# Kernel tuning notes

Measured on AMD Instinct MI355X. Metric: run time of the kernel, lower is better.

Reference implementation:

```python
import jax, jax.numpy as jnp
import numpy as np

N, E_RAW, IN_DIM, OUT_DIM, HEADS, EDGE_DIM = 20000, 320000, 64, 64, 4, 1
NEG_SLOPE = 0.2  # PyG GATv2 default negative_slope
LN_EPS = 1e-5


def setup_inputs() -> dict:
    key = jax.random.key(0)
    ks = jax.random.split(key, 14)
    HD = HEADS * OUT_DIM
    s_in = 1.0 / np.sqrt(IN_DIM)
    s_hd = 1.0 / np.sqrt(HD)
    return {
        "x": jax.random.normal(ks[0], (N, IN_DIM), dtype=jnp.float32),
        "edge_index": jax.random.randint(ks[1], (2, E_RAW), 0, N, dtype=jnp.int64),
        "edge_attr": jax.random.normal(ks[2], (E_RAW, EDGE_DIM), dtype=jnp.float32),
        # GATv2Conv params: lin_l, lin_r (with bias), lin_edge (no bias), att, final bias
        "W_l": jax.random.normal(ks[3], (IN_DIM, HD), dtype=jnp.float32) * s_in,
        "b_l": jnp.zeros((HD,), dtype=jnp.float32),
        "W_r": jax.random.normal(ks[4], (IN_DIM, HD), dtype=jnp.float32) * s_in,
        "b_r": jnp.zeros((HD,), dtype=jnp.float32),
        "W_e": jax.random.normal(ks[5], (EDGE_DIM, HD), dtype=jnp.float32),
        "att": jax.random.normal(ks[6], (HEADS, OUT_DIM), dtype=jnp.float32) * (1.0 / np.sqrt(OUT_DIM)),
        "bias_conv": jnp.zeros((HD,), dtype=jnp.float32),
        # proj: Linear(heads*out_dim -> out_dim)
        "W_p": jax.random.normal(ks[7], (HD, OUT_DIM), dtype=jnp.float32) * s_hd,
        "b_p": jnp.zeros((OUT_DIM,), dtype=jnp.float32),
        # LayerNorm(out_dim)
        "gamma": jnp.ones((OUT_DIM,), dtype=jnp.float32),
        "beta": jnp.zeros((OUT_DIM,), dtype=jnp.float32),
    }


def _gat_block(x, edge_index, edge_attr, W_l, b_l, W_r, b_r, W_e, att,
               bias_conv, W_p, b_p, gamma, beta):
    n = x.shape[0]
    H, D = att.shape
    # add self loops; edge_attr for loops = mean of existing (fill_value='mean')
    loop = jnp.arange(n)
    src = jnp.concatenate([edge_index[0], loop])
    dst = jnp.concatenate([edge_index[1], loop])
    ea_mean = jnp.mean(edge_attr, axis=0, keepdims=True)
    ea = jnp.concatenate([edge_attr, jnp.broadcast_to(ea_mean, (n, edge_attr.shape[1]))], axis=0)
    # node transforms: [N, H, D]
    x_l = (x @ W_l + b_l).reshape(n, H, D)
    x_r = (x @ W_r + b_r).reshape(n, H, D)
    e_feat = (ea @ W_e).reshape(-1, H, D)          # [Etot, H, D]
    # GATv2 attention logits per edge/head
    m = jax.nn.leaky_relu(x_l[src] + x_r[dst] + e_feat, NEG_SLOPE)
    logits = jnp.einsum('ehd,hd->eh', m, att)      # [Etot, H]
    # scatter-softmax over incoming edges of each target node
    lmax = jax.ops.segment_max(logits, dst, num_segments=n)
    lmax = jnp.where(jnp.isfinite(lmax), lmax, 0.0)
    ex = jnp.exp(logits - lmax[dst])
    den = jax.ops.segment_sum(ex, dst, num_segments=n)
    alpha = ex / (den[dst] + 1e-16)                # [Etot, H]
    # aggregate: sum_j alpha_ij * x_l[j]
    out = jax.ops.segment_sum(alpha[:, :, None] * x_l[src], dst, num_segments=n)
    h = out.reshape(n, H * D) + bias_conv
    # proj + residual + ELU + LayerNorm (dropout inactive in eval)
    h = h @ W_p + b_p
    h = h + x
    h = jax.nn.elu(h)
    mu = jnp.mean(h, axis=-1, keepdims=True)
    var = jnp.mean(jnp.square(h - mu), axis=-1, keepdims=True)
    return (h - mu) * jax.lax.rsqrt(var + LN_EPS) * gamma + beta


def reference(x, edge_index, edge_attr, W_l, b_l, W_r, b_r, W_e, att,
              bias_conv, W_p, b_p, gamma, beta):
    return _gat_block(x, edge_index, edge_attr, W_l, b_l, W_r, b_r, W_e, att,
                      bias_conv, W_p, b_p, gamma, beta)
```

## Files before the change

### kernel.cpp

```cpp
#include <hip/hip_runtime.h>
#include <math.h>

typedef _Float16 h2 __attribute__((ext_vector_type(2)));
typedef _Float16 h4 __attribute__((ext_vector_type(4)));
typedef _Float16 h8 __attribute__((ext_vector_type(8)));
typedef float f8 __attribute__((ext_vector_type(8)));

#define NEG_SLOPE 0.2f
#define LN_EPS 1e-5f
#define RESCALE_THR 8.0f
#define SLOT 64

#if __has_builtin(__builtin_amdgcn_fdot2)
#define FDOT2(a, b, c) __builtin_amdgcn_fdot2((a), (b), (c), false)
#else
static __device__ __forceinline__ float FDOT2(h2 a, h2 b, float c) {
    return c + (float)a[0] * (float)b[0] + (float)a[1] * (float)b[1];
}
#endif

static __device__ __forceinline__ float red8_dpp(float p) {
    p += __int_as_float(__builtin_amdgcn_mov_dpp(__float_as_int(p), 0xB1, 0xF, 0xF, true));
    p += __int_as_float(__builtin_amdgcn_mov_dpp(__float_as_int(p), 0x4E, 0xF, 0xF, true));
    p += __int_as_float(__builtin_amdgcn_mov_dpp(__float_as_int(p), 0x141, 0xF, 0xF, true));
    return p;
}

static __device__ __forceinline__ _Float16 f16_bits(unsigned short u) {
    union { unsigned short u; _Float16 h; } c; c.u = u; return c.h;
}
static __device__ __forceinline__ unsigned short bits_f16(_Float16 h) {
    union { unsigned short u; _Float16 h; } c; c.h = h; return c.u;
}

__global__ void init_kernel(int* __restrict__ cursor, float* __restrict__ partials,
                            float* __restrict__ easum, int n, int eb) {
    int i = blockIdx.x * 256 + threadIdx.x;
    if (i < n) cursor[i] = 0;
    if (i < eb) partials[i] = 0.f;
    if (i == 0) easum[0] = 0.f;
}

__global__ __launch_bounds__(256) void fill_kernel(
    const int* __restrict__ ei, const float* __restrict__ ea,
    int* __restrict__ cursor, unsigned int* __restrict__ rec,
    float* __restrict__ partials, int E) {
    int i = blockIdx.x * 256 + threadIdx.x;
    float s = 0.f;
    if (i < E) {
        int src = ei[i];
        int dst = ei[E + i];
        float a = ea[i];
        s = a;
        int pos = atomicAdd(&cursor[dst], 1);
        if (pos < SLOT) {
            unsigned int pk = ((unsigned int)bits_f16((_Float16)a) << 16) | (unsigned int)src;
            rec[(size_t)dst * SLOT + pos] = pk;
        }
    }
    __shared__ float red[4];
#pragma unroll
    for (int o = 32; o >= 1; o >>= 1) s += __shfl_xor(s, o);
    if ((threadIdx.x & 63) == 0) red[threadIdx.x >> 6] = s;
    __syncthreads();
    if (threadIdx.x == 0) partials[blockIdx.x] = red[0] + red[1] + red[2] + red[3];
}

__global__ __launch_bounds__(256) void transform_kernel(
    const float* __restrict__ x, const float* __restrict__ Wl, const float* __restrict__ bl,
    const float* __restrict__ Wr, const float* __restrict__ br,
    _Float16* __restrict__ xlh, _Float16* __restrict__ xrh,
    const float* __restrict__ partials, float* __restrict__ easum,
    int n, int eb, float inv_e) {
    __shared__ float xs[8][64];
    int nb = blockIdx.x * 8;
    int rows = n - nb; if (rows > 8) rows = 8;
    int t = threadIdx.x;
    if (t < rows * 16) ((float4*)xs)[t] = ((const float4*)(x + (size_t)nb * 64))[t];
    __syncthreads();
    float blv = bl[t], brv = br[t];
    float accl[8], accr[8];
#pragma unroll
    for (int i = 0; i < 8; ++i) { accl[i] = blv; accr[i] = brv; }
    for (int k = 0; k < 64; k += 4) {
        float wl0 = Wl[(k + 0) * 256 + t], wl1 = Wl[(k + 1) * 256 + t];
        float wl2 = Wl[(k + 2) * 256 + t], wl3 = Wl[(k + 3) * 256 + t];
        float wr0 = Wr[(k + 0) * 256 + t], wr1 = Wr[(k + 1) * 256 + t];
        float wr2 = Wr[(k + 2) * 256 + t], wr3 = Wr[(k + 3) * 256 + t];
#pragma unroll
        for (int i = 0; i < 8; ++i) {
            float4 xv = *(const float4*)&xs[i][k];
            accl[i] += xv.x * wl0 + xv.y * wl1 + xv.z * wl2 + xv.w * wl3;
            accr[i] += xv.x * wr0 + xv.y * wr1 + xv.z * wr2 + xv.w * wr3;
        }
    }
    for (int i = 0; i < rows; ++i) {
        xlh[(size_t)(nb + i) * 256 + t] = (_Float16)accl[i];
        xrh[(size_t)(nb + i) * 256 + t] = (_Float16)accr[i];
    }
    if (blockIdx.x == 0) {
        float s = 0.f;
        for (int i = t; i < eb; i += 256) s += partials[i];
#pragma unroll
        for (int o = 32; o >= 1; o >>= 1) s += __shfl_xor(s, o);
        __shared__ float red[4];
        if ((t & 63) == 0) red[t >> 6] = s;
        __syncthreads();
        if (t == 0) easum[0] = (red[0] + red[1] + red[2] + red[3]) * inv_e;
    }
}

__global__ __launch_bounds__(256) void gat_kernel(
    const _Float16* __restrict__ xlh, const _Float16* __restrict__ xrh,
    const int* __restrict__ cursor, const unsigned int* __restrict__ rec,
    const float* __restrict__ att, const float* __restrict__ We, const float* __restrict__ bias_conv,
    const float* __restrict__ easum, _Float16* __restrict__ hg, int n) {
    int wid = (blockIdx.x * blockDim.x + threadIdx.x) >> 6;
    if (wid >= n) return;
    int lane = threadIdx.x & 63;
    int half = lane >> 5, s = lane & 31;

    int pkv = (int)rec[(size_t)wid * SLOT + lane];
    int cnt = cursor[wid]; if (cnt > SLOT) cnt = SLOT;

    h8 xrv = ((const h8*)xrh)[(size_t)wid * 32 + s];
    h2 xr2[4], we2[4], c02 = {(_Float16)NEG_SLOPE, (_Float16)NEG_SLOPE};
    float atf[8];
    const float* attp = att + 8 * s;
    const float* wep = We + 8 * s;
#pragma unroll
    for (int j = 0; j < 4; ++j) {
        xr2[j] = (h2){xrv[2 * j], xrv[2 * j + 1]};
        we2[j] = (h2){(_Float16)wep[2 * j], (_Float16)wep[2 * j + 1]};
        atf[2 * j] = attp[2 * j]; atf[2 * j + 1] = attp[2 * j + 1];
    }
    const h8* xl8 = (const h8*)xlh;

    auto edge_p = [&](h8 v, _Float16 ah) -> float {
        h2 a2 = {ah, ah};
        float p = 0.f;
#pragma unroll
        for (int j = 0; j < 4; ++j) {
            h2 vj = (h2){v[2 * j], v[2 * j + 1]};
            h2 m = a2 * we2[j] + (vj + xr2[j]);
            h2 l = __builtin_elementwise_max(m, m * c02);
            p = fmaf((float)l[0], atf[2 * j], p);
            p = fmaf((float)l[1], atf[2 * j + 1], p);
        }
        return red8_dpp(p);
    };

    float M = -1e30f, S = 0.f;
    f8 accv = (f8)0.f;

#define ACC_FMA(V, W)                                        \
    _Pragma("unroll")                                        \
    for (int j = 0; j < 8; ++j) accv[j] = fmaf((float)(V)[j], (W), accv[j]);

#define ONLINE(P, V) {                                       \
        float newM = fmaxf(M, (P));                          \
        float sc = __expf(M - newM), w = __expf((P) - newM); \
        S = S * sc + w;                                      \
        accv *= sc;                                          \
        ACC_FMA(V, w);                                       \
        M = newM; }

#define LOADE(D, R)                                                         \
    int pk##D = __shfl(pkv, (R) + 2 * (D) + half);                          \
    h8 v##D = xl8[(size_t)(unsigned)(pk##D & 0xFFFF) * 32 + s];
#define PCOMP(D) float p##D = edge_p(v##D, f16_bits((unsigned short)((unsigned)pk##D >> 16)));

    {
        int pk0 = __shfl(pkv, 0);
        int src = wid;
        _Float16 ah = (_Float16)easum[0];
        if (half == 1 && cnt >= 1) {
            src = pk0 & 0xFFFF;
            ah = f16_bits((unsigned short)((unsigned)pk0 >> 16));
        }
        h8 v = xl8[(size_t)src * 32 + s];
        float p = edge_p(v, ah);
        if (half == 0 || cnt >= 1) {
            M = p; S = 1.f;
#pragma unroll
            for (int j = 0; j < 8; ++j) accv[j] = (float)v[j];
        }
    }
    int r = 1;
    for (; r + 15 < cnt; r += 16) {
        LOADE(0, r) LOADE(1, r) LOADE(2, r) LOADE(3, r)
        LOADE(4, r) LOADE(5, r) LOADE(6, r) LOADE(7, r)
        PCOMP(0) PCOMP(1) PCOMP(2) PCOMP(3)
        PCOMP(4) PCOMP(5) PCOMP(6) PCOMP(7)
        float pm = fmaxf(fmaxf(fmaxf(p0, p1), fmaxf(p2, p3)),
                         fmaxf(fmaxf(p4, p5), fmaxf(p6, p7)));
        if (__all(pm <= M + RESCALE_THR)) {
            float w0 = __expf(p0 - M), w1 = __expf(p1 - M);
            float w2 = __expf(p2 - M), w3 = __expf(p3 - M);
            float w4 = __expf(p4 - M), w5 = __expf(p5 - M);
            float w6 = __expf(p6 - M), w7 = __expf(p7 - M);
            S += ((w0 + w1) + (w2 + w3)) + ((w4 + w5) + (w6 + w7));
            ACC_FMA(v0, w0); ACC_FMA(v1, w1); ACC_FMA(v2, w2); ACC_FMA(v3, w3);
            ACC_FMA(v4, w4); ACC_FMA(v5, w5); ACC_FMA(v6, w6); ACC_FMA(v7, w7);
        } else {
            ONLINE(p0, v0); ONLINE(p1, v1); ONLINE(p2, v2); ONLINE(p3, v3);
            ONLINE(p4, v4); ONLINE(p5, v5); ONLINE(p6, v6); ONLINE(p7, v7);
        }
    }
    for (; r + 7 < cnt; r += 8) {
        LOADE(0, r) LOADE(1, r) LOADE(2, r) LOADE(3, r)
        PCOMP(0) PCOMP(1) PCOMP(2) PCOMP(3)
        float pm = fmaxf(fmaxf(p0, p1), fmaxf(p2, p3));
        if (__all(pm <= M + RESCALE_THR)) {
            float w0 = __expf(p0 - M), w1 = __expf(p1 - M);
            float w2 = __expf(p2 - M), w3 = __expf(p3 - M);
            S += (w0 + w1) + (w2 + w3);
            ACC_FMA(v0, w0); ACC_FMA(v1, w1); ACC_FMA(v2, w2); ACC_FMA(v3, w3);
        } else {
            ONLINE(p0, v0); ONLINE(p1, v1); ONLINE(p2, v2); ONLINE(p3, v3);
        }
    }
    for (; r + 1 < cnt; r += 2) {
        int pk0 = __shfl(pkv, r + half);
        h8 v0 = xl8[(size_t)(unsigned)(pk0 & 0xFFFF) * 32 + s];
        PCOMP(0)
        ONLINE(p0, v0);
    }
    if (r < cnt) {
        int pk0 = __shfl(pkv, r);
        h8 v0 = xl8[(size_t)(unsigned)(pk0 & 0xFFFF) * 32 + s];
        float p0 = edge_p(v0, f16_bits((unsigned short)((unsigned)pk0 >> 16)));
        if (half == 0) ONLINE(p0, v0);
    }

    float Mo = __shfl_xor(M, 32);
    float newM = fmaxf(M, Mo);
    float sc = __expf(M - newM);
    S *= sc;
    S += __shfl_xor(S, 32);
    accv *= sc;
#pragma unroll
    for (int j = 0; j < 8; ++j) accv[j] += __shfl_xor(accv[j], 32);
    float inv = 1.f / (S + 1e-16f);

    float4 bc = ((const float4*)bias_conv)[2 * s + half];
    int jb = 4 * half;
    h4 ov = {(_Float16)(accv[jb + 0] * inv + bc.x), (_Float16)(accv[jb + 1] * inv + bc.y),
             (_Float16)(accv[jb + 2] * inv + bc.z), (_Float16)(accv[jb + 3] * inv + bc.w)};
    ((h4*)hg)[(size_t)wid * 64 + 2 * s + half] = ov;
#undef ACC_FMA
#undef ONLINE
#undef LOADE
#undef PCOMP
}

__global__ __launch_bounds__(256) void proj_ln_kernel(
    const _Float16* __restrict__ hg, const float* __restrict__ Wp, const float* __restrict__ bp,
    const float* __restrict__ x, const float* __restrict__ gamma, const float* __restrict__ beta,
    float* __restrict__ out, int n) {
    __shared__ _Float16 wp_t[64 * 256];
    __shared__ _Float16 hs[32][264];
    int t = threadIdx.x;
    int nb = blockIdx.x * 32;
    for (int idx = t; idx < 4096; idx += 256) {
        float4 wv = ((const float4*)Wp)[idx];
        int k = idx >> 4, c0s = (idx & 15) * 4;
#pragma unroll
        for (int m = 0; m < 4; ++m) {
            int c = c0s + m;
            int off = c * 256 + ((((k >> 3) ^ ((c >> 2) & 7)) << 3) | (k & 7));
            wp_t[off] = (_Float16)((&wv.x)[m]);
        }
    }
    for (int idx = t; idx < 1024; idx += 256) {
        int row = idx >> 5, c8 = idx & 31;
        h8 hv = (h8)(_Float16)0.f;
        if (nb + row < n) hv = ((const h8*)hg)[(size_t)(nb + row) * 32 + c8];
        *(h8*)&hs[row][c8 * 8] = hv;
    }
    __syncthreads();

    int ng = t >> 4, cg = t & 15;
    int n0 = ng * 2, c0 = cg * 4;
    float acc[2][4];
#pragma unroll
    for (int a = 0; a < 2; ++a)
#pragma unroll
        for (int c = 0; c < 4; ++c) acc[a][c] = 0.f;

    for (int k = 0; k < 256; k += 8) {
        h8 hr[2], wr_[4];
#pragma unroll
        for (int a = 0; a < 2; ++a) hr[a] = *(const h8*)&hs[n0 + a][k];
#pragma unroll
        for (int j = 0; j < 4; ++j) {
            int c = c0 + j;
            int off = c * 256 + (((k >> 3) ^ ((c >> 2) & 7)) << 3);
            wr_[j] = *(const h8*)&wp_t[off];
        }
#pragma unroll
        for (int a = 0; a < 2; ++a) {
            const h2* hp = (const h2*)&hr[a];
#pragma unroll
            for (int j = 0; j < 4; ++j) {
                const h2* wp2 = (const h2*)&wr_[j];
                acc[a][j] = FDOT2(hp[0], wp2[0], acc[a][j]);
                acc[a][j] = FDOT2(hp[1], wp2[1], acc[a][j]);
                acc[a][j] = FDOT2(hp[2], wp2[2], acc[a][j]);
                acc[a][j] = FDOT2(hp[3], wp2[3], acc[a][j]);
            }
        }
    }

    float4 bpv = ((const float4*)bp)[cg];
    float4 gv  = ((const float4*)gamma)[cg];
    float4 bv  = ((const float4*)beta)[cg];
#pragma unroll
    for (int a = 0; a < 2; ++a) {
        int node = nb + n0 + a;
        float4 xv = make_float4(0.f, 0.f, 0.f, 0.f);
        if (node < n) xv = ((const float4*)x)[(size_t)node * 16 + cg];
        float h[4];
        h[0] = acc[a][0] + bpv.x + xv.x; h[1] = acc[a][1] + bpv.y + xv.y;
        h[2] = acc[a][2] + bpv.z + xv.z; h[3] = acc[a][3] + bpv.w + xv.w;
#pragma unroll
        for (int c = 0; c < 4; ++c) h[c] = h[c] > 0.f ? h[c] : expm1f(h[c]);
        float sum = h[0] + h[1] + h[2] + h[3];
#pragma unroll
        for (int o = 8; o >= 1; o >>= 1) sum += __shfl_xor(sum, o);
        float mu = sum * (1.f / 64.f);
        float d[4]; float s2 = 0.f;
#pragma unroll
        for (int c = 0; c < 4; ++c) { d[c] = h[c] - mu; s2 += d[c] * d[c]; }
#pragma unroll
        for (int o = 8; o >= 1; o >>= 1) s2 += __shfl_xor(s2, o);
        float r = rsqrtf(s2 * (1.f / 64.f) + LN_EPS);
        float4 ov;
        ov.x = d[0] * r * gv.x + bv.x; ov.y = d[1] * r * gv.y + bv.y;
        ov.z = d[2] * r * gv.z + bv.z; ov.w = d[3] * r * gv.w + bv.w;
        if (node < n) ((float4*)out)[(size_t)node * 16 + cg] = ov;
    }
}

extern "C" void kernel_launch(void* const* d_in, const int* in_sizes, int n_in,
                              void* d_out, int out_size, void* d_ws, size_t ws_size,
                              hipStream_t stream) {
    const float* x         = (const float*)d_in[0];
    const int*   ei        = (const int*)d_in[1];
    const float* ea        = (const float*)d_in[2];
    const float* Wl        = (const float*)d_in[3];
    const float* bl        = (const float*)d_in[4];
    const float* Wr        = (const float*)d_in[5];
    const float* br        = (const float*)d_in[6];
    const float* We        = (const float*)d_in[7];
    const float* att       = (const float*)d_in[8];
    const float* bias_conv = (const float*)d_in[9];
    const float* Wp        = (const float*)d_in[10];
    const float* bp        = (const float*)d_in[11];
    const float* gamma     = (const float*)d_in[12];
    const float* beta      = (const float*)d_in[13];
    float* out = (float*)d_out;

    int N = in_sizes[0] / 64;
    int E = in_sizes[2];
    int EB = (E + 255) / 256;

    char* w = (char*)d_ws;
    auto alloc = [&](size_t bytes) {
        char* p = w;
        w += (bytes + 255) & ~(size_t)255;
        return p;
    };
    _Float16*     xlh     = (_Float16*)    alloc((size_t)N * 256 * 2);
    _Float16*     xrh     = (_Float16*)    alloc((size_t)N * 256 * 2);
    _Float16*     hgh     = (_Float16*)    alloc((size_t)N * 256 * 2);
    unsigned int* rec     = (unsigned int*)alloc((size_t)N * SLOT * 4);
    int*          cursor  = (int*)         alloc((size_t)N * 4);
    float*        partials= (float*)       alloc((size_t)EB * 4);
    float*        easum   = (float*)       alloc(4);

    init_kernel<<<(N + 255) / 256, 256, 0, stream>>>(cursor, partials, easum, N, EB);
    fill_kernel<<<EB, 256, 0, stream>>>(ei, ea, cursor, rec, partials, E);
    transform_kernel<<<(N + 7) / 8, 256, 0, stream>>>(x, Wl, bl, Wr, br, xlh, xrh,
                                                      partials, easum, N, EB, 1.f / (float)E);
    gat_kernel<<<(N + 3) / 4, 256, 0, stream>>>(xlh, xrh, cursor, rec, att, We,
                                                bias_conv, easum, hgh, N);
    proj_ln_kernel<<<(N + 31) / 32, 256, 0, stream>>>(hgh, Wp, bp, x, gamma, beta, out, N);
}
```

Baseline: 108.2 us.

## Merge edge fill and node transform into one launch; widen proj block

The edge-bucketing fill and the node linear transform are independent, so they now run as one kernel whose blocks pick a role by block index. This lets both run at once instead of back to back. The edge_attr mean reduction moves into a small single-block kernel. The projection/LayerNorm kernel now uses 512 threads and 64 rows per block, which halves how often Wp is reloaded into LDS per row but needs more LDS per block. The proj compute section is not shown, so whether it was adapted to 512 threads cannot be checked.

```diff
diff --git a/kernel.cpp b/kernel.cpp
--- a/kernel.cpp
+++ b/kernel.cpp
@@ -33,81 +33,79 @@
     union { unsigned short u; _Float16 h; } c; c.h = h; return c.u;
 }
 
-__global__ void init_kernel(int* __restrict__ cursor, float* __restrict__ partials,
-                            float* __restrict__ easum, int n, int eb) {
+__global__ void init_kernel(int* __restrict__ cursor, int n) {
     int i = blockIdx.x * 256 + threadIdx.x;
     if (i < n) cursor[i] = 0;
-    if (i < eb) partials[i] = 0.f;
-    if (i == 0) easum[0] = 0.f;
-}
-
-__global__ __launch_bounds__(256) void fill_kernel(
+}
+
+__global__ __launch_bounds__(256) void prep_kernel(
     const int* __restrict__ ei, const float* __restrict__ ea,
-    int* __restrict__ cursor, unsigned int* __restrict__ rec,
-    float* __restrict__ partials, int E) {
-    int i = blockIdx.x * 256 + threadIdx.x;
-    float s = 0.f;
-    if (i < E) {
-        int src = ei[i];
-        int dst = ei[E + i];
-        float a = ea[i];
-        s = a;
-        int pos = atomicAdd(&cursor[dst], 1);
-        if (pos < SLOT) {
-            unsigned int pk = ((unsigned int)bits_f16((_Float16)a) << 16) | (unsigned int)src;
-            rec[(size_t)dst * SLOT + pos] = pk;
-        }
-    }
-    __shared__ float red[4];
-#pragma unroll
-    for (int o = 32; o >= 1; o >>= 1) s += __shfl_xor(s, o);
-    if ((threadIdx.x & 63) == 0) red[threadIdx.x >> 6] = s;
-    __syncthreads();
-    if (threadIdx.x == 0) partials[blockIdx.x] = red[0] + red[1] + red[2] + red[3];
-}
-
-__global__ __launch_bounds__(256) void transform_kernel(
+    int* __restrict__ cursor, unsigned int* __restrict__ rec, float* __restrict__ partials,
     const float* __restrict__ x, const float* __restrict__ Wl, const float* __restrict__ bl,
     const float* __restrict__ Wr, const float* __restrict__ br,
     _Float16* __restrict__ xlh, _Float16* __restrict__ xrh,
-    const float* __restrict__ partials, float* __restrict__ easum,
-    int n, int eb, float inv_e) {
-    __shared__ float xs[8][64];
-    int nb = blockIdx.x * 8;
-    int rows = n - nb; if (rows > 8) rows = 8;
-    int t = threadIdx.x;
-    if (t < rows * 16) ((float4*)xs)[t] = ((const float4*)(x + (size_t)nb * 64))[t];
-    __syncthreads();
-    float blv = bl[t], brv = br[t];
-    float accl[8], accr[8];
-#pragma unroll
-    for (int i = 0; i < 8; ++i) { accl[i] = blv; accr[i] = brv; }
-    for (int k = 0; k < 64; k += 4) {
-        float wl0 = Wl[(k + 0) * 256 + t], wl1 = Wl[(k + 1) * 256 + t];
-        float wl2 = Wl[(k + 2) * 256 + t], wl3 = Wl[(k + 3) * 256 + t];
-        float wr0 = Wr[(k + 0) * 256 + t], wr1 = Wr[(k + 1) * 256 + t];
-        float wr2 = Wr[(k + 2) * 256 + t], wr3 = Wr[(k + 3) * 256 + t];
-#pragma unroll
-        for (int i = 0; i < 8; ++i) {
-            float4 xv = *(const float4*)&xs[i][k];
-            accl[i] += xv.x * wl0 + xv.y * wl1 + xv.z * wl2 + xv.w * wl3;
-            accr[i] += xv.x * wr0 + xv.y * wr1 + xv.z * wr2 + xv.w * wr3;
-        }
-    }
-    for (int i = 0; i < rows; ++i) {
-        xlh[(size_t)(nb + i) * 256 + t] = (_Float16)accl[i];
-        xrh[(size_t)(nb + i) * 256 + t] = (_Float16)accr[i];
-    }
-    if (blockIdx.x == 0) {
+    int N, int E, int EB) {
+    int b = blockIdx.x, t = threadIdx.x;
+    if (b < EB) {
+        int i = b * 256 + t;
         float s = 0.f;
-        for (int i = t; i < eb; i += 256) s += partials[i];
+        if (i < E) {
+            int src = ei[i];
+            int dst = ei[E + i];
+            float a = ea[i];
+            s = a;
+            int pos = atomicAdd(&cursor[dst], 1);
+            if (pos < SLOT) {
+                unsigned int pk = ((unsigned int)bits_f16((_Float16)a) << 16) | (unsigned int)src;
+                rec[(size_t)dst * SLOT + pos] = pk;
+            }
+        }
+        __shared__ float red[4];
 #pragma unroll
         for (int o = 32; o >= 1; o >>= 1) s += __shfl_xor(s, o);
-        __shared__ float red[4];
         if ((t & 63) == 0) red[t >> 6] = s;
         __syncthreads();
-        if (t == 0) easum[0] = (red[0] + red[1] + red[2] + red[3]) * inv_e;
-    }
+        if (t == 0) partials[b] = red[0] + red[1] + red[2] + red[3];
+    } else {
+        __shared__ float xs[8][64];
+        int nb = (b - EB) * 8;
+        int rows = N - nb; if (rows > 8) rows = 8;
+        if (rows <= 0) return;
+        if (t < rows * 16) ((float4*)xs)[t] = ((const float4*)(x + (size_t)nb * 64))[t];
+        __syncthreads();
+        float blv = bl[t], brv = br[t];
+        float accl[8], accr[8];
+#pragma unroll
+        for (int i = 0; i < 8; ++i) { accl[i] = blv; accr[i] = brv; }
+        for (int k = 0; k < 64; k += 4) {
+            float wl0 = Wl[(k + 0) * 256 + t], wl1 = Wl[(k + 1) * 256 + t];
+            float wl2 = Wl[(k + 2) * 256 + t], wl3 = Wl[(k + 3) * 256 + t];
+            float wr0 = Wr[(k + 0) * 256 + t], wr1 = Wr[(k + 1) * 256 + t];
+            float wr2 = Wr[(k + 2) * 256 + t], wr3 = Wr[(k + 3) * 256 + t];
+#pragma unroll
+            for (int i = 0; i < 8; ++i) {
+                float4 xv = *(const float4*)&xs[i][k];
+                accl[i] += xv.x * wl0 + xv.y * wl1 + xv.z * wl2 + xv.w * wl3;
+                accr[i] += xv.x * wr0 + xv.y * wr1 + xv.z * wr2 + xv.w * wr3;
+            }
+        }
+        for (int i = 0; i < rows; ++i) {
+            xlh[(size_t)(nb + i) * 256 + t] = (_Float16)accl[i];
+            xrh[(size_t)(nb + i) * 256 + t] = (_Float16)accr[i];
+        }
+    }
+}
+
+__global__ __launch_bounds__(256) void easum_kernel(const float* __restrict__ partials,
+                                                    float* __restrict__ easum, int eb, float inv_e) {
+    float s = 0.f;
+    for (int i = threadIdx.x; i < eb; i += 256) s += partials[i];
+#pragma unroll
+    for (int o = 32; o >= 1; o >>= 1) s += __shfl_xor(s, o);
+    __shared__ float red[4];
+    if ((threadIdx.x & 63) == 0) red[threadIdx.x >> 6] = s;
+    __syncthreads();
+    if (threadIdx.x == 0) easum[0] = (red[0] + red[1] + red[2] + red[3]) * inv_e;
 }
 
 __global__ __launch_bounds__(256) void gat_kernel(
@@ -254,15 +252,15 @@
 #undef PCOMP
 }
 
-__global__ __launch_bounds__(256) void proj_ln_kernel(
+__global__ __launch_bounds__(512) void proj_ln_kernel(
     const _Float16* __restrict__ hg, const float* __restrict__ Wp, const float* __restrict__ bp,
     const float* __restrict__ x, const float* __restrict__ gamma, const float* __restrict__ beta,
     float* __restrict__ out, int n) {
     __shared__ _Float16 wp_t[64 * 256];
-    __shared__ _Float16 hs[32][264];
+    __shared__ _Float16 hs[64][264];
     int t = threadIdx.x;
-    int nb = blockIdx.x * 32;
-    for (int idx = t; idx < 4096; idx += 256) {
+    int nb = blockIdx.x * 64;
+    for (int idx = t; idx < 4096; idx += 512) {
         float4 wv = ((const float4*)Wp)[idx];
         int k = idx >> 4, c0s = (idx & 15) * 4;
 #pragma unroll
@@ -272,7 +270,7 @@
             wp_t[off] = (_Float16)((&wv.x)[m]);
         }
     }
-    for (int idx = t; idx < 1024; idx += 256) {
+    for (int idx = t; idx < 2048; idx += 512) {
         int row = idx >> 5, c8 = idx & 31;
         h8 hv = (h8)(_Float16)0.f;
         if (nb + row < n) hv = ((const h8*)hg)[(size_t)(nb + row) * 32 + c8];
@@ -364,6 +362,7 @@
     int N = in_sizes[0] / 64;
     int E = in_sizes[2];
     int EB = (E + 255) / 256;
+    int TB = (N + 7) / 8;
 
     char* w = (char*)d_ws;
     auto alloc = [&](size_t bytes) {
@@ -379,11 +378,11 @@
     float*        partials= (float*)       alloc((size_t)EB * 4);
     float*        easum   = (float*)       alloc(4);
 
-    init_kernel<<<(N + 255) / 256, 256, 0, stream>>>(cursor, partials, easum, N, EB);
-    fill_kernel<<<EB, 256, 0, stream>>>(ei, ea, cursor, rec, partials, E);
-    transform_kernel<<<(N + 7) / 8, 256, 0, stream>>>(x, Wl, bl, Wr, br, xlh, xrh,
-                                                      partials, easum, N, EB, 1.f / (float)E);
+    init_kernel<<<(N + 255) / 256, 256, 0, stream>>>(cursor, N);
+    prep_kernel<<<EB + TB, 256, 0, stream>>>(ei, ea, cursor, rec, partials,
+                                             x, Wl, bl, Wr, br, xlh, xrh, N, E, EB);
+    easum_kernel<<<1, 256, 0, stream>>>(partials, easum, EB, 1.f / (float)E);
     gat_kernel<<<(N + 3) / 4, 256, 0, stream>>>(xlh, xrh, cursor, rec, att, We,
                                                 bias_conv, easum, hgh, N);
-    proj_ln_kernel<<<(N + 31) / 32, 256, 0, stream>>>(hgh, Wp, bp, x, gamma, beta, out, N);
-}
+    proj_ln_kernel<<<(N + 63) / 64, 512, 0, stream>>>(hgh, Wp, bp, x, gamma, beta, out, N);
+}
```

After: 108.7 us. Within noise of the previous version (+0.4%).
